# Kernel optimization log

Hardware: AMD Instinct MI355X
Metric: run time of the kernel (lower is better)

## Reference

```python
import jax, jax.numpy as jnp
import numpy as np

DIM = 512
HID = DIM // 4        # cross-attention inner dim
MLP_HID = int(DIM * 2.0)
EPS = 1e-5


def _xavier(key, shape):
    fan_in, fan_out = shape[0], shape[1]
    limit = float(np.sqrt(6.0 / (fan_in + fan_out)))
    return jax.random.uniform(key, shape, jnp.float32, -limit, limit)


def setup_inputs() -> dict:
    key = jax.random.key(0)
    ks = jax.random.split(key, 12)
    n, v = 8, 2048
    x = jax.random.normal(ks[0], (n, v, DIM), jnp.float32)
    y = jax.random.normal(ks[1], (n, v, DIM), jnp.float32)
    Wq = _xavier(ks[2], (DIM, HID))
    Wk = _xavier(ks[3], (DIM, HID))
    Wv = _xavier(ks[4], (DIM, DIM))
    gamma = jnp.ones((DIM,), jnp.float32)
    beta = jnp.zeros((DIM,), jnp.float32)
    # nn.Linear default init: U(-1/sqrt(fan_in), 1/sqrt(fan_in))
    b1lim = 1.0 / np.sqrt(DIM)
    W1 = jax.random.uniform(ks[5], (DIM, MLP_HID), jnp.float32, -b1lim, b1lim)
    b1 = jax.random.uniform(ks[6], (MLP_HID,), jnp.float32, -b1lim, b1lim)
    b2lim = 1.0 / np.sqrt(MLP_HID)
    W2 = jax.random.uniform(ks[7], (MLP_HID, DIM), jnp.float32, -b2lim, b2lim)
    b2 = jax.random.uniform(ks[8], (DIM,), jnp.float32, -b2lim, b2lim)
    return {"x": x, "y": y, "Wq": Wq, "Wk": Wk, "Wv": Wv,
            "gamma": gamma, "beta": beta, "W1": W1, "b1": b1, "W2": W2, "b2": b2}


def _layernorm(x, gamma, beta):
    mu = jnp.mean(x, axis=-1, keepdims=True)
    var = jnp.var(x, axis=-1, keepdims=True)
    return (x - mu) * jax.lax.rsqrt(var + EPS) * gamma + beta


def reference(x, y, Wq, Wk, Wv, gamma, beta, W1, b1, W2, b2):
    scale = HID ** (-0.5)
    q = jnp.einsum('nvc,co->nvo', x, Wq)          # [n, q, HID]
    k = jnp.einsum('nvc,co->nvo', y, Wk)          # [n, k, HID]
    v = jnp.einsum('nvc,co->nvo', y, Wv)          # [n, k, DIM]
    attn = jax.nn.softmax(jnp.einsum('nqc,nkc->nqk', q, k) * scale, axis=-1)
    x = x + jnp.einsum('nqk,nkc->nqc', attn, v)   # residual + attention
    h = _layernorm(x, gamma, beta)
    h = jax.nn.gelu(h @ W1 + b1, approximate=False) @ W2 + b2
    return x + h
```

## Files before the change

### kernel.cpp

```cpp
#include <hip/hip_runtime.h>
#include <cstddef>
#include <cstdint>

typedef __attribute__((ext_vector_type(8))) short short8;
typedef __attribute__((ext_vector_type(4))) short s16x4;
typedef __attribute__((ext_vector_type(4))) float f32x4;
typedef __attribute__((ext_vector_type(16))) float f32x16;

#define GLOAD_LDS16(gp, lp) __builtin_amdgcn_global_load_lds( \
    (const __attribute__((address_space(1))) void*)(gp),      \
    (__attribute__((address_space(3))) void*)(lp), 16, 0, 0)

__device__ __forceinline__ short f2bf(float f) {
    union { float f; unsigned u; } v; v.f = f;
    unsigned r = v.u + 0x7fffu + ((v.u >> 16) & 1u);
    return (short)(r >> 16);
}

__device__ __forceinline__ void transpose_tile_f32(
    const float* __restrict__ in, short* __restrict__ out,
    int R, int C, int ty, int tx)
{
    __shared__ short tile[64][68];
    int r0 = ty * 64, c0 = tx * 64;
    int t = threadIdx.x, tr = t >> 6, tc = t & 63;
#pragma unroll
    for (int i = 0; i < 16; ++i) {
        int r = i * 4 + tr;
        tile[r][tc] = f2bf(in[(size_t)(r0 + r) * C + (c0 + tc)]);
    }
    __syncthreads();
#pragma unroll
    for (int i = 0; i < 16; ++i) {
        int r = i * 4 + tr;
        out[(size_t)(c0 + r) * R + (r0 + tc)] = tile[tc][r];
    }
}

__global__ __launch_bounds__(256) void prep_kernel(
    const float* __restrict__ x, const float* __restrict__ y,
    const float* __restrict__ Wq, const float* __restrict__ Wk,
    const float* __restrict__ Wv, const float* __restrict__ W1,
    const float* __restrict__ W2,
    short* xb, short* yb,
    short* WqT, short* WkT, short* WvT, short* W1T, short* W2T)
{
    int bid = blockIdx.x, t = threadIdx.x;
    if (bid < 8192) {
        size_t e = ((size_t)bid << 11) + (size_t)t * 8;
        const float* src; short* dst; size_t o2;
        if (e < 8388608) { src = x; dst = xb; o2 = e; }
        else             { src = y; dst = yb; o2 = e - 8388608; }
        f32x4 a = *(const f32x4*)(src + o2);
        f32x4 b = *(const f32x4*)(src + o2 + 4);
        short8 v;
        v[0] = f2bf(a[0]); v[1] = f2bf(a[1]); v[2] = f2bf(a[2]); v[3] = f2bf(a[3]);
        v[4] = f2bf(b[0]); v[5] = f2bf(b[1]); v[6] = f2bf(b[2]); v[7] = f2bf(b[3]);
        *(short8*)(dst + o2) = v;
        return;
    }
    int b2 = bid - 8192;
    const float* in; short* out; int R, C;
    if (b2 < 16)       { in = Wq; out = WqT; R = 512;  C = 128; }
    else if (b2 < 32)  { in = Wk; out = WkT; R = 512;  C = 128;  b2 -= 16; }
    else if (b2 < 96)  { in = Wv; out = WvT; R = 512;  C = 512;  b2 -= 32; }
    else if (b2 < 224) { in = W1; out = W1T; R = 512;  C = 1024; b2 -= 96; }
    else               { in = W2; out = W2T; R = 1024; C = 512;  b2 -= 224; }
    int nx = C >> 6;
    transpose_tile_f32(in, out, R, C, b2 / nx, b2 % nx);
}

__global__ __launch_bounds__(256, 2) void proj_gemm(
    const short* __restrict__ xb, const short* __restrict__ yb,
    const short* __restrict__ WqT, const short* __restrict__ WkT,
    const short* __restrict__ WvT,
    short* __restrict__ qbf, short* __restrict__ kbff, short* __restrict__ vbf)
{
    __shared__ short As[128][64];
    __shared__ short Bs[128][64];
    int bid = blockIdx.x;
    const short* A; const short* BT; short* outp; int n0, N, mode, mb;
    if (bid < 128)      { A = xb; BT = WqT; outp = qbf;  n0 = 0; N = 128; mode = 0; mb = bid; }
    else if (bid < 256) { A = yb; BT = WkT; outp = kbff; n0 = 0; N = 128; mode = 0; mb = bid - 128; }
    else { int v2 = bid - 256; A = yb; BT = WvT; outp = vbf; n0 = (v2 & 3) << 7; N = 512; mode = 1; mb = v2 >> 2; }
    const int m0 = mb << 7;
    const int K = 512;
    const int t = threadIdx.x, l = t & 63, w = t >> 6;
    const int wm = w >> 1, wn = w & 1;
    const int lo = l & 15, hi = l >> 4;

    f32x4 acc[4][4] = {};
    const int srow = l >> 3;
    const int scg  = (l & 7) ^ (srow & 7);

    for (int kt = 0; kt < K; kt += 64) {
#pragma unroll
        for (int i = 0; i < 4; ++i) {
            int seg = w * 4 + i;
            int row = seg * 8 + srow;
            GLOAD_LDS16(A + (size_t)(m0 + row) * K + kt + scg * 8, &As[seg * 8][0]);
        }
#pragma unroll
        for (int i = 0; i < 4; ++i) {
            int seg = w * 4 + i;
            int row = seg * 8 + srow;
            GLOAD_LDS16(BT + (size_t)(n0 + row) * K + kt + scg * 8, &Bs[seg * 8][0]);
        }
        __syncthreads();
#pragma unroll
        for (int kk = 0; kk < 2; ++kk) {
            short8 af[4], bfv[4];
            const int rc = ((kk * 4 + hi) ^ (lo & 7)) * 8;
#pragma unroll
            for (int mi = 0; mi < 4; ++mi)
                af[mi] = *(const short8*)&As[wm * 64 + mi * 16 + lo][rc];
#pragma unroll
            for (int ni = 0; ni < 4; ++ni)
                bfv[ni] = *(const short8*)&Bs[wn * 64 + ni * 16 + lo][rc];
            __builtin_amdgcn_s_setprio(1);
#pragma unroll
            for (int mi = 0; mi < 4; ++mi)
#pragma unroll
                for (int ni = 0; ni < 4; ++ni)
                    acc[mi][ni] = __builtin_amdgcn_mfma_f32_16x16x32_bf16(
                        af[mi], bfv[ni], acc[mi][ni], 0, 0, 0);
            __builtin_amdgcn_s_setprio(0);
        }
        __syncthreads();
    }

    if (mode == 0) {
#pragma unroll
        for (int mi = 0; mi < 4; ++mi) {
#pragma unroll
            for (int ni = 0; ni < 4; ++ni) {
                int rowb = m0 + wm * 64 + mi * 16 + hi * 4;
                int col  = n0 + wn * 64 + ni * 16 + lo;
                size_t base = ((size_t)(rowb >> 5) * (N >> 4) + (col >> 4)) * 512
                            + ((col & 15) >> 3) * 256 + (rowb & 31) * 8 + (col & 7);
#pragma unroll
                for (int r = 0; r < 4; ++r)
                    outp[base + r * 8] = f2bf(acc[mi][ni][r]);
            }
        }
    } else {
#pragma unroll
        for (int mi = 0; mi < 4; ++mi) {
#pragma unroll
            for (int ni = 0; ni < 4; ++ni) {
                int rowb = m0 + wm * 64 + mi * 16 + hi * 4;
                int col  = n0 + wn * 64 + ni * 16 + lo;
                size_t base = ((size_t)(rowb >> 4) * (N >> 5) + (col >> 5)) * 512
                            + ((rowb & 15) >> 3) * 256 + (col & 31) * 8 + (rowb & 7);
                s16x4 pk;
#pragma unroll
                for (int r = 0; r < 4; ++r) pk[r] = f2bf(acc[mi][ni][r]);
                *(s16x4*)(outp + base) = pk;
            }
        }
    }
}

template<int EPI>
__global__ __launch_bounds__(256, 2) void gemm_kernel(
    const short* __restrict__ A, const short* __restrict__ BT, void* outv,
    const float* __restrict__ bias, const float* __restrict__ resid,
    int N, int K)
{
    __shared__ short As[128][64];
    __shared__ short Bs[128][64];
    int bid = blockIdx.x;
    const int cpx = gridDim.x >> 3;
    bid = (bid & 7) * cpx + (bid >> 3);
    const int nb = N >> 7;
    const int m0 = (bid / nb) << 7;
    const int n0 = (bid % nb) << 7;
    const int t = threadIdx.x, l = t & 63, w = t >> 6;
    const int wm = w >> 1, wn = w & 1;
    const int lo = l & 15, hi = l >> 4;

    f32x4 acc[4][4] = {};
    const int srow = l >> 3;
    const int scg  = (l & 7) ^ (srow & 7);

    for (int kt = 0; kt < K; kt += 64) {
#pragma unroll
        for (int i = 0; i < 4; ++i) {
            int seg = w * 4 + i;
            int row = seg * 8 + srow;
            GLOAD_LDS16(A + (size_t)(m0 + row) * K + kt + scg * 8, &As[seg * 8][0]);
        }
#pragma unroll
        for (int i = 0; i < 4; ++i) {
            int seg = w * 4 + i;
            int row = seg * 8 + srow;
            GLOAD_LDS16(BT + (size_t)(n0 + row) * K + kt + scg * 8, &Bs[seg * 8][0]);
        }
        __syncthreads();
#pragma unroll
        for (int kk = 0; kk < 2; ++kk) {
            short8 af[4], bfv[4];
            const int rc = ((kk * 4 + hi) ^ (lo & 7)) * 8;
#pragma unroll
            for (int mi = 0; mi < 4; ++mi)
                af[mi] = *(const short8*)&As[wm * 64 + mi * 16 + lo][rc];
#pragma unroll
            for (int ni = 0; ni < 4; ++ni)
                bfv[ni] = *(const short8*)&Bs[wn * 64 + ni * 16 + lo][rc];
            __builtin_amdgcn_s_setprio(1);
#pragma unroll
            for (int mi = 0; mi < 4; ++mi)
#pragma unroll
                for (int ni = 0; ni < 4; ++ni)
                    acc[mi][ni] = __builtin_amdgcn_mfma_f32_16x16x32_bf16(
                        af[mi], bfv[ni], acc[mi][ni], 0, 0, 0);
            __builtin_amdgcn_s_setprio(0);
        }
        __syncthreads();
    }

#pragma unroll
    for (int mi = 0; mi < 4; ++mi) {
#pragma unroll
        for (int ni = 0; ni < 4; ++ni) {
#pragma unroll
            for (int r = 0; r < 4; ++r) {
                int row = m0 + wm * 64 + mi * 16 + hi * 4 + r;
                int col = n0 + wn * 64 + ni * 16 + lo;
                size_t idx = (size_t)row * N + col;
                float v = acc[mi][ni][r];
                if (EPI == 2) {
                    v += bias[col];
                    v = 0.5f * v * (1.0f + erff(v * 0.70710678118654752f));
                    ((short*)outv)[idx] = f2bf(v);
                } else {
                    v += bias[col] + resid[idx];
                    ((float*)outv)[idx] = v;
                }
            }
        }
    }
}

__global__ __launch_bounds__(512, 2) void flash_kernel(
    const float* __restrict__ x,
    const short* __restrict__ qbf,
    const short* __restrict__ kbff,
    const short* __restrict__ vbf,
    float* __restrict__ xres)
{
    __shared__ short Ps[2][8][512];
    __shared__ float mpart[8][32];
    __shared__ float lpart[8][32];

    const int bid = blockIdx.x;
    const int n = bid & 7;
    const int qtile = bid >> 3;
    const int q0 = qtile << 6;
    const int t = threadIdx.x, l = t & 63, w = t >> 6;
    const int qh = w >> 2, kq = w & 3;
    const int lo5 = l & 31, hi2 = l >> 5;
    const float C1 = 0.08838834764831845f * 1.4426950408889634f;
    const float THR = 90.509668f;

    short8 qf[8];
    {
        const short* qp = qbf + (((size_t)(n * 64 + qtile * 2 + qh) * 8) << 9) + l * 8;
#pragma unroll
        for (int s = 0; s < 8; ++s) qf[s] = *(const short8*)(qp + (s << 9));
    }

    f32x16 o00 = {}, o01 = {}, o10 = {}, o11 = {};
    float m0 = -1e30f, m1 = -1e30f, lp = 0.f;

    const short* kb0 = kbff + (((size_t)(n * 64) * 8) << 9);
    const short* vb0 = vbf + ((((size_t)(n * 128)) * 16 + w * 2) << 9);

    for (int kt = 0; kt < 2048; kt += 128) {
        const short* kp = kb0 + (((size_t)((kt >> 5) + kq) * 8) << 9) + l * 8;
        short8 kf[8];
#pragma unroll
        for (int s = 0; s < 8; ++s) kf[s] = *(const short8*)(kp + (s << 9));

        f32x16 sacc = {};
        __builtin_amdgcn_s_setprio(1);
#pragma unroll
        for (int s = 0; s < 8; ++s)
            sacc = __builtin_amdgcn_mfma_f32_32x32x16_bf16(kf[s], qf[s], sacc, 0, 0, 0);
        __builtin_amdgcn_s_setprio(0);

        short8 vf[16];
        {
            const short* vp = vb0 + (((size_t)(kt >> 4) * 16) << 9) + l * 8;
#pragma unroll
            for (int ks = 0; ks < 8; ++ks)
#pragma unroll
                for (int nb = 0; nb < 2; ++nb)
                    vf[ks * 2 + nb] = *(const short8*)(vp + (((size_t)(ks * 16 + nb)) << 9));
        }

        float lmax = sacc[0];
#pragma unroll
        for (int r = 1; r < 16; ++r) lmax = fmaxf(lmax, sacc[r]);
        lmax = fmaxf(lmax, __shfl_xor(lmax, 32));
        if (l < 32) mpart[w][l] = lmax;
        __syncthreads();

        float nm0 = fmaxf(fmaxf(mpart[0][lo5], mpart[1][lo5]),
                          fmaxf(mpart[2][lo5], mpart[3][lo5]));
        float nm1 = fmaxf(fmaxf(mpart[4][lo5], mpart[5][lo5]),
                          fmaxf(mpart[6][lo5], mpart[7][lo5]));
        float t0 = (nm0 > m0 + THR) ? nm0 : m0;
        float t1 = (nm1 > m1 + THR) ? nm1 : m1;
        float a0 = exp2f((m0 - t0) * C1);
        float a1 = exp2f((m1 - t1) * C1);
        m0 = t0; m1 = t1;

        const float mC1 = (qh ? m1 : m0) * C1;
        float lsum = 0.f;
#pragma unroll
        for (int r = 0; r < 16; ++r) {
            float p = exp2f(fmaf(sacc[r], C1, -mC1));
            sacc[r] = p; lsum += p;
        }
        lp = lp * (qh ? a1 : a0) + lsum;

        {
            int wq[8], sx[8];
#pragma unroll
            for (int q2 = 0; q2 < 8; ++q2) {
                int a;
                asm("v_cvt_pk_bf16_f32 %0, %1, %2"
                    : "=v"(a) : "v"(sacc[2 * q2]), "v"(sacc[2 * q2 + 1]));
                wq[q2] = a;
            }
#pragma unroll
            for (int q2 = 0; q2 < 8; ++q2) sx[q2] = __shfl_xor(wq[q2], 32);
            union { int i[4]; short8 v; } u0, u1;
            u0.i[0] = hi2 ? sx[2] : wq[0];
            u0.i[1] = hi2 ? sx[3] : wq[1];
            u0.i[2] = hi2 ? wq[2] : sx[0];
            u0.i[3] = hi2 ? wq[3] : sx[1];
            u1.i[0] = hi2 ? sx[6] : wq[4];
            u1.i[1] = hi2 ? sx[7] : wq[5];
            u1.i[2] = hi2 ? wq[6] : sx[4];
            u1.i[3] = hi2 ? wq[7] : sx[5];
            *(short8*)&Ps[qh][kq * 2][l * 8]     = u0.v;
            *(short8*)&Ps[qh][kq * 2 + 1][l * 8] = u1.v;
        }
        __syncthreads();

        if (!(__all(a0 == 1.f) & __all(a1 == 1.f))) {
#pragma unroll
            for (int r = 0; r < 16; ++r) {
                int qr = (r & 3) + 8 * (r >> 2) + 4 * hi2;
                float ar0 = __shfl(a0, qr);
                float ar1 = __shfl(a1, qr);
                o00[r] *= ar0; o01[r] *= ar0;
                o10[r] *= ar1; o11[r] *= ar1;
            }
        }
        __builtin_amdgcn_s_setprio(1);
#pragma unroll
        for (int ks = 0; ks < 8; ++ks) {
            short8 p0 = *(const short8*)&Ps[0][ks][l * 8];
            short8 p1 = *(const short8*)&Ps[1][ks][l * 8];
            o00 = __builtin_amdgcn_mfma_f32_32x32x16_bf16(p0, vf[ks * 2 + 0], o00, 0, 0, 0);
            o01 = __builtin_amdgcn_mfma_f32_32x32x16_bf16(p0, vf[ks * 2 + 1], o01, 0, 0, 0);
            o10 = __builtin_amdgcn_mfma_f32_32x32x16_bf16(p1, vf[ks * 2 + 0], o10, 0, 0, 0);
            o11 = __builtin_amdgcn_mfma_f32_32x32x16_bf16(p1, vf[ks * 2 + 1], o11, 0, 0, 0);
        }
        __builtin_amdgcn_s_setprio(0);
    }

    float l2 = lp + __shfl_xor(lp, 32);
    if (l < 32) lpart[w][l] = l2;
    __syncthreads();
    float li0 = 1.f / (lpart[0][lo5] + lpart[1][lo5] + lpart[2][lo5] + lpart[3][lo5]);
    float li1 = 1.f / (lpart[4][lo5] + lpart[5][lo5] + lpart[6][lo5] + lpart[7][lo5]);
#pragma unroll
    for (int r = 0; r < 16; ++r) {
        int qr = (r & 3) + 8 * (r >> 2) + 4 * hi2;
        float ir0 = __shfl(li0, qr);
        float ir1 = __shfl(li1, qr);
        int row0 = q0 + qr, row1 = q0 + 32 + qr;
        size_t b0 = ((size_t)(n * 2048 + row0) << 9) + w * 64 + lo5;
        size_t b1 = ((size_t)(n * 2048 + row1) << 9) + w * 64 + lo5;
        xres[b0]      = x[b0]      + o00[r] * ir0;
        xres[b0 + 32] = x[b0 + 32] + o01[r] * ir0;
        xres[b1]      = x[b1]      + o10[r] * ir1;
        xres[b1 + 32] = x[b1 + 32] + o11[r] * ir1;
    }
}

__global__ __launch_bounds__(256) void ln_kernel(
    const float* __restrict__ xr, const float* __restrict__ gamma,
    const float* __restrict__ beta, short* __restrict__ hb)
{
    int row = (blockIdx.x << 2) + (threadIdx.x >> 6);
    int lane = threadIdx.x & 63;
    const float* p = xr + ((size_t)row << 9) + lane * 8;
    f32x4 a = *(const f32x4*)p;
    f32x4 b = *(const f32x4*)(p + 4);
    float s = a[0] + a[1] + a[2] + a[3] + b[0] + b[1] + b[2] + b[3];
#pragma unroll
    for (int m = 1; m < 64; m <<= 1) s += __shfl_xor(s, m);
    float mu = s * (1.0f / 512.0f);
    float q = 0.f;
#pragma unroll
    for (int j = 0; j < 4; ++j) { float d = a[j] - mu; q += d * d; }
#pragma unroll
    for (int j = 0; j < 4; ++j) { float d = b[j] - mu; q += d * d; }
#pragma unroll
    for (int m = 1; m < 64; m <<= 1) q += __shfl_xor(q, m);
    float rs = rsqrtf(q * (1.0f / 512.0f) + 1e-5f);
    f32x4 g0 = *(const f32x4*)(gamma + lane * 8);
    f32x4 g1 = *(const f32x4*)(gamma + lane * 8 + 4);
    f32x4 e0 = *(const f32x4*)(beta + lane * 8);
    f32x4 e1 = *(const f32x4*)(beta + lane * 8 + 4);
    short8 ov;
#pragma unroll
    for (int j = 0; j < 4; ++j) ov[j]     = f2bf((a[j] - mu) * rs * g0[j] + e0[j]);
#pragma unroll
    for (int j = 0; j < 4; ++j) ov[4 + j] = f2bf((b[j] - mu) * rs * g1[j] + e1[j]);
    *(short8*)(hb + ((size_t)row << 9) + lane * 8) = ov;
}

extern "C" void kernel_launch(void* const* d_in, const int* in_sizes, int n_in,
                              void* d_out, int out_size, void* d_ws, size_t ws_size,
                              hipStream_t stream)
{
    const float* x     = (const float*)d_in[0];
    const float* y     = (const float*)d_in[1];
    const float* Wq    = (const float*)d_in[2];
    const float* Wk    = (const float*)d_in[3];
    const float* Wv    = (const float*)d_in[4];
    const float* gamma = (const float*)d_in[5];
    const float* beta  = (const float*)d_in[6];
    const float* W1    = (const float*)d_in[7];
    const float* b1    = (const float*)d_in[8];
    const float* W2    = (const float*)d_in[9];
    const float* b2    = (const float*)d_in[10];
    float* out = (float*)d_out;

    char* ws = (char*)d_ws;
    size_t off = 0;
    auto alloc = [&](size_t bytes) -> void* {
        void* p = ws + off;
        off += (bytes + 255) & ~(size_t)255;
        return p;
    };
    short* WqT  = (short*)alloc((size_t)128 * 512 * 2);
    short* WkT  = (short*)alloc((size_t)128 * 512 * 2);
    short* WvT  = (short*)alloc((size_t)512 * 512 * 2);
    short* W1T  = (short*)alloc((size_t)1024 * 512 * 2);
    short* W2T  = (short*)alloc((size_t)512 * 1024 * 2);
    short* qbf  = (short*)alloc((size_t)16384 * 128 * 2);
    short* kbff = (short*)alloc((size_t)16384 * 128 * 2);
    short* vbf  = (short*)alloc((size_t)16384 * 512 * 2);
    short* xb   = (short*)alloc((size_t)16384 * 512 * 2);
    short* hb   = xb;
    short* yb   = (short*)alloc((size_t)16384 * 512 * 2);
    short* gb   = (short*)alloc((size_t)16384 * 1024 * 2);

    prep_kernel<<<8544, 256, 0, stream>>>(x, y, Wq, Wk, Wv, W1, W2,
                                          xb, yb, WqT, WkT, WvT, W1T, W2T);
    proj_gemm<<<768, 256, 0, stream>>>(xb, yb, WqT, WkT, WvT, qbf, kbff, vbf);
    flash_kernel<<<256, 512, 0, stream>>>(x, qbf, kbff, vbf, out);
    ln_kernel<<<4096, 256, 0, stream>>>(out, gamma, beta, hb);
    gemm_kernel<2><<<1024, 256, 0, stream>>>(hb, W1T, gb, b1, nullptr, 1024, 512);
    gemm_kernel<3><<<512,  256, 0, stream>>>(gb, W2T, out, b2, out, 512, 1024);

    (void)in_sizes; (void)n_in; (void)out_size; (void)ws_size;
}
```

Before: 179.6 us.

## Software-pipeline QK softmax with PV in flash kernel and fuse LayerNorm epilogue

Restructures the flash attention loop so the QK^T scores and softmax for the next key tile are computed while the PV MMAs for the current tile run. P tiles and the max partials are double-buffered in shared memory, which leaves one barrier per iteration instead of two, and V loads are split into two halves. LayerNorm is also fused into the flash epilogue through block-level row sum and sum-of-squares reductions, which removes the separate ln_kernel launch and its re-read of the residual. The cost is more registers and shared memory, and variance is now computed as E[x^2]-mu^2, which is less numerically robust.

```diff
diff --git a/kernel.cpp b/kernel.cpp
--- a/kernel.cpp
+++ b/kernel.cpp
@@ -247,11 +247,17 @@
     const short* __restrict__ qbf,
     const short* __restrict__ kbff,
     const short* __restrict__ vbf,
-    float* __restrict__ xres)
+    float* __restrict__ xres,
+    const float* __restrict__ gamma,
+    const float* __restrict__ beta,
+    short* __restrict__ hb)
 {
-    __shared__ short Ps[2][8][512];
-    __shared__ float mpart[8][32];
+    __shared__ short Ps[2][2][8][512];
+    __shared__ float mpart[2][8][32];
     __shared__ float lpart[8][32];
+    __shared__ float rsum[8][64];
+    __shared__ float rsq[8][64];
+    __shared__ float murs[2][64];
 
     const int bid = blockIdx.x;
     const int n = bid & 7;
@@ -272,66 +278,160 @@
 
     f32x16 o00 = {}, o01 = {}, o10 = {}, o11 = {};
     float m0 = -1e30f, m1 = -1e30f, lp = 0.f;
+    float ac0 = 0.f, ac1 = 0.f;
 
     const short* kb0 = kbff + (((size_t)(n * 64) * 8) << 9);
     const short* vb0 = vbf + ((((size_t)(n * 128)) * 16 + w * 2) << 9);
 
-    for (int kt = 0; kt < 2048; kt += 128) {
-        const short* kp = kb0 + (((size_t)((kt >> 5) + kq) * 8) << 9) + l * 8;
+    {
+        const short* kp = kb0 + (((size_t)kq * 8) << 9) + l * 8;
         short8 kf[8];
 #pragma unroll
         for (int s = 0; s < 8; ++s) kf[s] = *(const short8*)(kp + (s << 9));
-
-        f32x16 sacc = {};
+        f32x16 sa = {};
         __builtin_amdgcn_s_setprio(1);
 #pragma unroll
         for (int s = 0; s < 8; ++s)
-            sacc = __builtin_amdgcn_mfma_f32_32x32x16_bf16(kf[s], qf[s], sacc, 0, 0, 0);
+            sa = __builtin_amdgcn_mfma_f32_32x32x16_bf16(kf[s], qf[s], sa, 0, 0, 0);
         __builtin_amdgcn_s_setprio(0);
-
-        short8 vf[16];
-        {
-            const short* vp = vb0 + (((size_t)(kt >> 4) * 16) << 9) + l * 8;
-#pragma unroll
-            for (int ks = 0; ks < 8; ++ks)
-#pragma unroll
-                for (int nb = 0; nb < 2; ++nb)
-                    vf[ks * 2 + nb] = *(const short8*)(vp + (((size_t)(ks * 16 + nb)) << 9));
-        }
-
-        float lmax = sacc[0];
-#pragma unroll
-        for (int r = 1; r < 16; ++r) lmax = fmaxf(lmax, sacc[r]);
+        float lmax = sa[0];
+#pragma unroll
+        for (int r = 1; r < 16; ++r) lmax = fmaxf(lmax, sa[r]);
         lmax = fmaxf(lmax, __shfl_xor(lmax, 32));
-        if (l < 32) mpart[w][l] = lmax;
+        if (l < 32) mpart[0][w][l] = lmax;
         __syncthreads();
-
-        float nm0 = fmaxf(fmaxf(mpart[0][lo5], mpart[1][lo5]),
-                          fmaxf(mpart[2][lo5], mpart[3][lo5]));
-        float nm1 = fmaxf(fmaxf(mpart[4][lo5], mpart[5][lo5]),
-                          fmaxf(mpart[6][lo5], mpart[7][lo5]));
-        float t0 = (nm0 > m0 + THR) ? nm0 : m0;
-        float t1 = (nm1 > m1 + THR) ? nm1 : m1;
-        float a0 = exp2f((m0 - t0) * C1);
-        float a1 = exp2f((m1 - t1) * C1);
-        m0 = t0; m1 = t1;
-
+        m0 = fmaxf(fmaxf(mpart[0][0][lo5], mpart[0][1][lo5]),
+                   fmaxf(mpart[0][2][lo5], mpart[0][3][lo5]));
+        m1 = fmaxf(fmaxf(mpart[0][4][lo5], mpart[0][5][lo5]),
+                   fmaxf(mpart[0][6][lo5], mpart[0][7][lo5]));
         const float mC1 = (qh ? m1 : m0) * C1;
         float lsum = 0.f;
 #pragma unroll
         for (int r = 0; r < 16; ++r) {
-            float p = exp2f(fmaf(sacc[r], C1, -mC1));
-            sacc[r] = p; lsum += p;
-        }
-        lp = lp * (qh ? a1 : a0) + lsum;
-
-        {
+            float p = exp2f(fmaf(sa[r], C1, -mC1));
+            sa[r] = p; lsum += p;
+        }
+        lp = lsum;
+        int wq[8], sx[8];
+#pragma unroll
+        for (int q2 = 0; q2 < 8; ++q2) {
+            int a;
+            asm("v_cvt_pk_bf16_f32 %0, %1, %2"
+                : "=v"(a) : "v"(sa[2 * q2]), "v"(sa[2 * q2 + 1]));
+            wq[q2] = a;
+        }
+#pragma unroll
+        for (int q2 = 0; q2 < 8; ++q2) sx[q2] = __shfl_xor(wq[q2], 32);
+        union { int i[4]; short8 v; } u0, u1;
+        u0.i[0] = hi2 ? sx[2] : wq[0];
+        u0.i[1] = hi2 ? sx[3] : wq[1];
+        u0.i[2] = hi2 ? wq[2] : sx[0];
+        u0.i[3] = hi2 ? wq[3] : sx[1];
+        u1.i[0] = hi2 ? sx[6] : wq[4];
+        u1.i[1] = hi2 ? sx[7] : wq[5];
+        u1.i[2] = hi2 ? wq[6] : sx[4];
+        u1.i[3] = hi2 ? wq[7] : sx[5];
+        *(short8*)&Ps[0][qh][kq * 2][l * 8]     = u0.v;
+        *(short8*)&Ps[0][qh][kq * 2 + 1][l * 8] = u1.v;
+    }
+
+    for (int kt2 = 0; kt2 < 16; ++kt2) {
+        const bool hn = kt2 < 15;
+        const short* vp = vb0 + (((size_t)(kt2 * 128)) << 9) + l * 8;
+
+        short8 vfa[8];
+#pragma unroll
+        for (int p = 0; p < 8; ++p)
+            vfa[p] = *(const short8*)(vp + (((size_t)((p >> 1) * 16 + (p & 1))) << 9));
+
+        f32x16 sa;
+        float an0 = 1.f, an1 = 1.f;
+        if (hn) {
+            const short* kp = kb0 + (((size_t)((kt2 + 1) * 4 + kq) * 8) << 9) + l * 8;
+            short8 kf[8];
+#pragma unroll
+            for (int s = 0; s < 8; ++s) kf[s] = *(const short8*)(kp + (s << 9));
+            f32x16 z = {};
+            sa = z;
+            __builtin_amdgcn_s_setprio(1);
+#pragma unroll
+            for (int s = 0; s < 8; ++s)
+                sa = __builtin_amdgcn_mfma_f32_32x32x16_bf16(kf[s], qf[s], sa, 0, 0, 0);
+            __builtin_amdgcn_s_setprio(0);
+            float lmax = sa[0];
+#pragma unroll
+            for (int r = 1; r < 16; ++r) lmax = fmaxf(lmax, sa[r]);
+            lmax = fmaxf(lmax, __shfl_xor(lmax, 32));
+            if (l < 32) mpart[(kt2 + 1) & 1][w][l] = lmax;
+        }
+        __syncthreads();
+
+        short8 vfb[8];
+#pragma unroll
+        for (int p = 0; p < 8; ++p)
+            vfb[p] = *(const short8*)(vp + (((size_t)((4 + (p >> 1)) * 16 + (p & 1))) << 9));
+
+        if (hn) {
+            const int mb = (kt2 + 1) & 1;
+            float nm0 = fmaxf(fmaxf(mpart[mb][0][lo5], mpart[mb][1][lo5]),
+                              fmaxf(mpart[mb][2][lo5], mpart[mb][3][lo5]));
+            float nm1 = fmaxf(fmaxf(mpart[mb][4][lo5], mpart[mb][5][lo5]),
+                              fmaxf(mpart[mb][6][lo5], mpart[mb][7][lo5]));
+            float t0 = (nm0 > m0 + THR) ? nm0 : m0;
+            float t1 = (nm1 > m1 + THR) ? nm1 : m1;
+            an0 = exp2f((m0 - t0) * C1);
+            an1 = exp2f((m1 - t1) * C1);
+            m0 = t0; m1 = t1;
+            const float mC1 = (qh ? m1 : m0) * C1;
+            float lsum = 0.f;
+#pragma unroll
+            for (int r = 0; r < 16; ++r) {
+                float p = exp2f(fmaf(sa[r], C1, -mC1));
+                sa[r] = p; lsum += p;
+            }
+            lp = lp * (qh ? an1 : an0) + lsum;
+        }
+
+        if (!(__all(ac0 == 1.f) & __all(ac1 == 1.f))) {
+#pragma unroll
+            for (int r = 0; r < 16; ++r) {
+                int qr = (r & 3) + 8 * (r >> 2) + 4 * hi2;
+                float ar0 = __shfl(ac0, qr);
+                float ar1 = __shfl(ac1, qr);
+                o00[r] *= ar0; o01[r] *= ar0;
+                o10[r] *= ar1; o11[r] *= ar1;
+            }
+        }
+
+        const int pb = kt2 & 1;
+        __builtin_amdgcn_s_setprio(1);
+#pragma unroll
+        for (int ks = 0; ks < 4; ++ks) {
+            short8 p0 = *(const short8*)&Ps[pb][0][ks][l * 8];
+            short8 p1 = *(const short8*)&Ps[pb][1][ks][l * 8];
+            o00 = __builtin_amdgcn_mfma_f32_32x32x16_bf16(p0, vfa[ks * 2 + 0], o00, 0, 0, 0);
+            o01 = __builtin_amdgcn_mfma_f32_32x32x16_bf16(p0, vfa[ks * 2 + 1], o01, 0, 0, 0);
+            o10 = __builtin_amdgcn_mfma_f32_32x32x16_bf16(p1, vfa[ks * 2 + 0], o10, 0, 0, 0);
+            o11 = __builtin_amdgcn_mfma_f32_32x32x16_bf16(p1, vfa[ks * 2 + 1], o11, 0, 0, 0);
+        }
+#pragma unroll
+        for (int ks = 4; ks < 8; ++ks) {
+            short8 p0 = *(const short8*)&Ps[pb][0][ks][l * 8];
+            short8 p1 = *(const short8*)&Ps[pb][1][ks][l * 8];
+            o00 = __builtin_amdgcn_mfma_f32_32x32x16_bf16(p0, vfb[(ks - 4) * 2 + 0], o00, 0, 0, 0);
+            o01 = __builtin_amdgcn_mfma_f32_32x32x16_bf16(p0, vfb[(ks - 4) * 2 + 1], o01, 0, 0, 0);
+            o10 = __builtin_amdgcn_mfma_f32_32x32x16_bf16(p1, vfb[(ks - 4) * 2 + 0], o10, 0, 0, 0);
+            o11 = __builtin_amdgcn_mfma_f32_32x32x16_bf16(p1, vfb[(ks - 4) * 2 + 1], o11, 0, 0, 0);
+        }
+        __builtin_amdgcn_s_setprio(0);
+
+        if (hn) {
             int wq[8], sx[8];
 #pragma unroll
             for (int q2 = 0; q2 < 8; ++q2) {
                 int a;
                 asm("v_cvt_pk_bf16_f32 %0, %1, %2"
-                    : "=v"(a) : "v"(sacc[2 * q2]), "v"(sacc[2 * q2 + 1]));
+                    : "=v"(a) : "v"(sa[2 * q2]), "v"(sa[2 * q2 + 1]));
                 wq[q2] = a;
             }
 #pragma unroll
@@ -345,32 +445,11 @@
             u1.i[1] = hi2 ? sx[7] : wq[5];
             u1.i[2] = hi2 ? wq[6] : sx[4];
             u1.i[3] = hi2 ? wq[7] : sx[5];
-            *(short8*)&Ps[qh][kq * 2][l * 8]     = u0.v;
-            *(short8*)&Ps[qh][kq * 2 + 1][l * 8] = u1.v;
-        }
-        __syncthreads();
-
-        if (!(__all(a0 == 1.f) & __all(a1 == 1.f))) {
-#pragma unroll
-            for (int r = 0; r < 16; ++r) {
-                int qr = (r & 3) + 8 * (r >> 2) + 4 * hi2;
-                float ar0 = __shfl(a0, qr);
-                float ar1 = __shfl(a1, qr);
-                o00[r] *= ar0; o01[r] *= ar0;
-                o10[r] *= ar1; o11[r] *= ar1;
-            }
-        }
-        __builtin_amdgcn_s_setprio(1);
-#pragma unroll
-        for (int ks = 0; ks < 8; ++ks) {
-            short8 p0 = *(const short8*)&Ps[0][ks][l * 8];
-            short8 p1 = *(const short8*)&Ps[1][ks][l * 8];
-            o00 = __builtin_amdgcn_mfma_f32_32x32x16_bf16(p0, vf[ks * 2 + 0], o00, 0, 0, 0);
-            o01 = __builtin_amdgcn_mfma_f32_32x32x16_bf16(p0, vf[ks * 2 + 1], o01, 0, 0, 0);
-            o10 = __builtin_amdgcn_mfma_f32_32x32x16_bf16(p1, vf[ks * 2 + 0], o10, 0, 0, 0);
-            o11 = __builtin_amdgcn_mfma_f32_32x32x16_bf16(p1, vf[ks * 2 + 1], o11, 0, 0, 0);
-        }
-        __builtin_amdgcn_s_setprio(0);
+            const int nb2 = (kt2 + 1) & 1;
+            *(short8*)&Ps[nb2][qh][kq * 2][l * 8]     = u0.v;
+            *(short8*)&Ps[nb2][qh][kq * 2 + 1][l * 8] = u1.v;
+            ac0 = an0; ac1 = an1;
+        }
     }
 
     float l2 = lp + __shfl_xor(lp, 32);
@@ -378,52 +457,58 @@
     __syncthreads();
     float li0 = 1.f / (lpart[0][lo5] + lpart[1][lo5] + lpart[2][lo5] + lpart[3][lo5]);
     float li1 = 1.f / (lpart[4][lo5] + lpart[5][lo5] + lpart[6][lo5] + lpart[7][lo5]);
+    const int c0 = w * 64 + lo5;
 #pragma unroll
     for (int r = 0; r < 16; ++r) {
         int qr = (r & 3) + 8 * (r >> 2) + 4 * hi2;
         float ir0 = __shfl(li0, qr);
         float ir1 = __shfl(li1, qr);
-        int row0 = q0 + qr, row1 = q0 + 32 + qr;
-        size_t b0 = ((size_t)(n * 2048 + row0) << 9) + w * 64 + lo5;
-        size_t b1 = ((size_t)(n * 2048 + row1) << 9) + w * 64 + lo5;
-        xres[b0]      = x[b0]      + o00[r] * ir0;
-        xres[b0 + 32] = x[b0 + 32] + o01[r] * ir0;
-        xres[b1]      = x[b1]      + o10[r] * ir1;
-        xres[b1 + 32] = x[b1 + 32] + o11[r] * ir1;
-    }
-}
-
-__global__ __launch_bounds__(256) void ln_kernel(
-    const float* __restrict__ xr, const float* __restrict__ gamma,
-    const float* __restrict__ beta, short* __restrict__ hb)
-{
-    int row = (blockIdx.x << 2) + (threadIdx.x >> 6);
-    int lane = threadIdx.x & 63;
-    const float* p = xr + ((size_t)row << 9) + lane * 8;
-    f32x4 a = *(const f32x4*)p;
-    f32x4 b = *(const f32x4*)(p + 4);
-    float s = a[0] + a[1] + a[2] + a[3] + b[0] + b[1] + b[2] + b[3];
-#pragma unroll
-    for (int m = 1; m < 64; m <<= 1) s += __shfl_xor(s, m);
-    float mu = s * (1.0f / 512.0f);
-    float q = 0.f;
-#pragma unroll
-    for (int j = 0; j < 4; ++j) { float d = a[j] - mu; q += d * d; }
-#pragma unroll
-    for (int j = 0; j < 4; ++j) { float d = b[j] - mu; q += d * d; }
-#pragma unroll
-    for (int m = 1; m < 64; m <<= 1) q += __shfl_xor(q, m);
-    float rs = rsqrtf(q * (1.0f / 512.0f) + 1e-5f);
-    f32x4 g0 = *(const f32x4*)(gamma + lane * 8);
-    f32x4 g1 = *(const f32x4*)(gamma + lane * 8 + 4);
-    f32x4 e0 = *(const f32x4*)(beta + lane * 8);
-    f32x4 e1 = *(const f32x4*)(beta + lane * 8 + 4);
-    short8 ov;
-#pragma unroll
-    for (int j = 0; j < 4; ++j) ov[j]     = f2bf((a[j] - mu) * rs * g0[j] + e0[j]);
-#pragma unroll
-    for (int j = 0; j < 4; ++j) ov[4 + j] = f2bf((b[j] - mu) * rs * g1[j] + e1[j]);
-    *(short8*)(hb + ((size_t)row << 9) + lane * 8) = ov;
+        size_t b0 = ((size_t)(n * 2048 + q0 + qr) << 9) + c0;
+        size_t b1 = ((size_t)(n * 2048 + q0 + 32 + qr) << 9) + c0;
+        float v00 = x[b0]      + o00[r] * ir0;
+        float v01 = x[b0 + 32] + o01[r] * ir0;
+        float v10 = x[b1]      + o10[r] * ir1;
+        float v11 = x[b1 + 32] + o11[r] * ir1;
+        xres[b0] = v00; xres[b0 + 32] = v01;
+        xres[b1] = v10; xres[b1 + 32] = v11;
+        o00[r] = v00; o01[r] = v01; o10[r] = v10; o11[r] = v11;
+        float s0 = v00 + v01, sq0 = v00 * v00 + v01 * v01;
+        float s1 = v10 + v11, sq1 = v10 * v10 + v11 * v11;
+#pragma unroll
+        for (int mm = 1; mm < 32; mm <<= 1) {
+            s0 += __shfl_xor(s0, mm); sq0 += __shfl_xor(sq0, mm);
+            s1 += __shfl_xor(s1, mm); sq1 += __shfl_xor(sq1, mm);
+        }
+        if (lo5 == 0) {
+            rsum[w][qr] = s0;      rsq[w][qr] = sq0;
+            rsum[w][32 + qr] = s1; rsq[w][32 + qr] = sq1;
+        }
+    }
+    __syncthreads();
+    if (t < 64) {
+        float s = 0.f, qq = 0.f;
+#pragma unroll
+        for (int ww = 0; ww < 8; ++ww) { s += rsum[ww][t]; qq += rsq[ww][t]; }
+        float mu = s * (1.0f / 512.0f);
+        float var = qq * (1.0f / 512.0f) - mu * mu;
+        murs[0][t] = mu;
+        murs[1][t] = rsqrtf(var + 1e-5f);
+    }
+    __syncthreads();
+    const float g0 = gamma[c0], g1 = gamma[c0 + 32];
+    const float e0 = beta[c0],  e1 = beta[c0 + 32];
+#pragma unroll
+    for (int r = 0; r < 16; ++r) {
+        int qr = (r & 3) + 8 * (r >> 2) + 4 * hi2;
+        float mu0 = murs[0][qr],      rs0 = murs[1][qr];
+        float mu1 = murs[0][32 + qr], rs1 = murs[1][32 + qr];
+        size_t h0 = ((size_t)(n * 2048 + q0 + qr) << 9) + c0;
+        size_t h1 = ((size_t)(n * 2048 + q0 + 32 + qr) << 9) + c0;
+        hb[h0]      = f2bf((o00[r] - mu0) * rs0 * g0 + e0);
+        hb[h0 + 32] = f2bf((o01[r] - mu0) * rs0 * g1 + e1);
+        hb[h1]      = f2bf((o10[r] - mu1) * rs1 * g0 + e0);
+        hb[h1 + 32] = f2bf((o11[r] - mu1) * rs1 * g1 + e1);
+    }
 }
 
 extern "C" void kernel_launch(void* const* d_in, const int* in_sizes, int n_in,
@@ -466,8 +551,7 @@
     prep_kernel<<<8544, 256, 0, stream>>>(x, y, Wq, Wk, Wv, W1, W2,
                                           xb, yb, WqT, WkT, WvT, W1T, W2T);
     proj_gemm<<<768, 256, 0, stream>>>(xb, yb, WqT, WkT, WvT, qbf, kbff, vbf);
-    flash_kernel<<<256, 512, 0, stream>>>(x, qbf, kbff, vbf, out);
-    ln_kernel<<<4096, 256, 0, stream>>>(out, gamma, beta, hb);
+    flash_kernel<<<256, 512, 0, stream>>>(x, qbf, kbff, vbf, out, gamma, beta, hb);
     gemm_kernel<2><<<1024, 256, 0, stream>>>(hb, W1T, gb, b1, nullptr, 1024, 512);
     gemm_kernel<3><<<512,  256, 0, stream>>>(gb, W2T, out, b2, out, 512, 1024);
 
```

After: 172.1 us. 4.2% less time.
